# Optimization experiments

Measured on AMD Instinct MI355X. Metric: run time of the kernel, lower is better.

Reference implementation:

```python
import jax, jax.numpy as jnp
from jax import lax
import numpy as np

SR = 48000
NUM_BANDS = 12
IR_LEN = 32768          # reverb impulse-response length in samples
NUM_TAPS = 511          # bandpass FIR length for the noise filterbank
BS, CHS, T = 32, 2, 131072
EPS = 1e-8


def make_filterbank():
    """12-band windowed-sinc bandpass filterbank spanning 0..Nyquist."""
    n = np.arange(NUM_TAPS) - (NUM_TAPS - 1) / 2.0
    win = np.hamming(NUM_TAPS)
    filts = []
    for b in range(NUM_BANDS):
        lo = 0.5 * b / NUM_BANDS
        hi = 0.5 * (b + 1) / NUM_BANDS
        h = 2.0 * hi * np.sinc(2.0 * hi * n) - 2.0 * lo * np.sinc(2.0 * lo * n)
        filts.append(h * win)
    return np.stack(filts).astype(np.float32)  # (12, NUM_TAPS)


def _distortion(x, drive_db):
    # tanh waveshaper with dB drive gain
    return jnp.tanh(x * 10.0 ** (drive_db / 20.0))


def _compressor(x, thr, ratio, atk_ms, rel_ms, knee, makeup):
    # soft-knee gain computer in dB domain
    x_db = 20.0 * jnp.log10(jnp.abs(x) + EPS)          # (bs, chs, T)
    knee = jnp.maximum(knee, 1e-3)
    over = x_db - thr
    g_knee = x_db + (1.0 / ratio - 1.0) * (over + knee / 2.0) ** 2 / (2.0 * knee)
    g = jnp.where(2.0 * over < -knee, x_db,
                  jnp.where(2.0 * over > knee, thr + over / ratio, g_knee))
    gain_db = g - x_db                                  # desired gain reduction (<= 0)
    # per-sample attack/release one-pole envelope follower (sequential scan)
    alpha_a = jnp.exp(-1.0 / (SR * atk_ms / 1000.0))
    alpha_r = jnp.exp(-1.0 / (SR * rel_ms / 1000.0))
    g_t = jnp.moveaxis(gain_db, -1, 0)                  # (T, bs, chs)

    def step(prev, cur):
        alpha = jnp.where(cur < prev, alpha_a, alpha_r)  # attack when reduction grows
        new = alpha * prev + (1.0 - alpha) * cur
        return new, new

    _, smooth = lax.scan(step, jnp.zeros(g_t.shape[1:], x.dtype), g_t)
    smooth = jnp.moveaxis(smooth, 0, -1)                # (bs, chs, T)
    return x * 10.0 ** ((smooth + makeup) / 20.0)


def _reverb(x, band_gains, band_decays, mix, noise, fir_bank):
    bs, chs, seq = x.shape
    n = noise.reshape(bs * chs, NUM_BANDS, -1)          # (N, 12, IR_LEN+TAPS-1)
    # grouped conv: each band of noise filtered by its bandpass FIR
    filt = lax.conv_general_dilated(
        n, fir_bank[:, None, :], (1,), 'VALID',
        dimension_numbers=('NCH', 'OIH', 'NCH'),
        feature_group_count=NUM_BANDS)                  # (N, 12, IR_LEN)
    t = jnp.linspace(0.0, 1.0, IR_LEN, dtype=x.dtype)
    d = band_decays * 10.0 + 1.0
    env = jnp.exp(-d[:, None] * t[None, :])             # (12, IR_LEN) decay envelopes
    ir = jnp.mean(filt * (env * band_gains[:, None]), axis=1)  # (N, IR_LEN)
    ir = ir.reshape(bs, chs, IR_LEN)
    # FFT convolution of input with the synthesized IR
    nfft = seq + IR_LEN - 1
    wet = jnp.fft.irfft(jnp.fft.rfft(x, nfft) * jnp.fft.rfft(ir, nfft), nfft)[..., :seq]
    return (1.0 - mix) * x + mix * wet


def _forward(x, drive, thr, ratio, atk, rel, knee, makeup, mix,
             band_gains, band_decays, noise, fir_bank):
    x = _distortion(x, drive)
    x = _compressor(x, thr, ratio, atk, rel, knee, makeup)
    return _reverb(x, band_gains, band_decays, mix, noise, fir_bank)


def setup_inputs() -> dict:
    key = jax.random.key(0)
    k1, k2 = jax.random.split(key)
    return {
        "x": 0.5 * jax.random.normal(k1, (BS, CHS, T), jnp.float32),
        "drive": jnp.float32(5.0),
        "threshold_db": jnp.float32(-20.0),
        "ratio": jnp.float32(4.0),
        "attack_ms": jnp.float32(10.0),
        "release_ms": jnp.float32(50.0),
        "knee_db": jnp.float32(6.0),
        "makeup_gain_db": jnp.float32(0.0),
        "mix": jnp.float32(0.3),
        "band_gains": jnp.zeros((NUM_BANDS,), jnp.float32),
        "band_decays": 0.5 * jnp.ones((NUM_BANDS,), jnp.float32),
        "noise": jax.random.normal(k2, (BS, CHS, NUM_BANDS, IR_LEN + NUM_TAPS - 1), jnp.float32),
        "fir_bank": jnp.asarray(make_filterbank()),
    }


def reference(x, drive, threshold_db, ratio, attack_ms, release_ms, knee_db,
              makeup_gain_db, mix, band_gains, band_decays, noise, fir_bank):
    return _forward(x, drive, threshold_db, ratio, attack_ms, release_ms,
                    knee_db, makeup_gain_db, mix, band_gains, band_decays,
                    noise, fir_bank)
```

## Files before the change

### kernel.cpp

```cpp
#include <hip/hip_runtime.h>
#include <math.h>
#include <stdint.h>

#define NCHW    64
#define TLEN    131072
#define IRLEN   32768
#define NTAPS   511
#define NBANDS  12
#define NOISELEN (IRLEN + NTAPS - 1)

#define WUP     4096
#define CHK     512
#define NBLK2   (TLEN / CHK)
#define NQ      (TLEN / 4)
#define GRP     16

#define K10     0.16609640474436813f
#define DB2     6.0205999132796239f

__device__ __forceinline__ float fast_tanh(float z) {
    float az = fabsf(z);
    float e  = exp2f(az * 2.8853900817779268f);
    float r  = 1.0f - 2.0f / (e + 1.0f);
    return copysignf(r, z);
}

__device__ __forceinline__ float gain_db_one(float xs, float g, float thr,
                                             float q, float knee, float inv2k) {
    float y    = fast_tanh(xs * g);
    float a    = fabsf(y) + 1e-8f;
    float xdb  = __log2f(a) * DB2;
    float over = xdb - thr;
    float h    = over + 0.5f * knee;
    float gk   = q * h * h * inv2k;
    float t2   = 2.0f * over;
    return (t2 < -knee) ? 0.0f : ((t2 > knee) ? q * over : gk);
}

__device__ __forceinline__ float f4c(const float4& v, int s) {
    return s == 0 ? v.x : (s == 1 ? v.y : (s == 2 ? v.z : v.w));
}

__global__ __launch_bounds__(256) void k1_gain(
    const float* __restrict__ x,
    const float* __restrict__ p_drive, const float* __restrict__ p_thr,
    const float* __restrict__ p_ratio, const float* __restrict__ p_knee,
    const float* __restrict__ p_atk,   const float* __restrict__ p_rel,
    const float* __restrict__ band_gains,
    float4* __restrict__ q4, float* __restrict__ q1, float4* __restrict__ pq,
    int* __restrict__ flag)
{
    if (blockIdx.x == 0 && threadIdx.x == 0) {
        int f = 0;
        #pragma unroll
        for (int b = 0; b < NBANDS; ++b) f |= (band_gains[b] != 0.0f) ? 1 : 0;
        *flag = f;
    }
    __shared__ float S[64 * 65];
    int t0 = blockIdx.x * 64;
    int l  = threadIdx.x & 63;
    int w  = threadIdx.x >> 6;

    float g     = exp2f(p_drive[0] * K10);
    float thr   = p_thr[0];
    float knee  = fmaxf(p_knee[0], 1e-3f);
    float qr    = 1.0f / p_ratio[0] - 1.0f;
    float inv2k = 1.0f / (2.0f * knee);
    float aa    = expf(-1.0f / (48.0f * p_atk[0]));
    float ar    = expf(-1.0f / (48.0f * p_rel[0]));
    float omaa  = 1.0f - aa;
    float rho   = (1.0f - ar) / omaa;

    #pragma unroll
    for (int i = 0; i < 16; ++i) {
        int ch = w * 16 + i;
        float xv = x[(size_t)ch * TLEN + t0 + l];
        S[l * 65 + ch] = omaa * gain_db_one(xv, g, thr, qr, knee, inv2k);
    }
    __syncthreads();

    int ch = threadIdx.x & 63;
    int ql = threadIdx.x >> 6;
    #pragma unroll
    for (int k = 0; k < 4; ++k) {
        int qq = ql * 4 + k;
        int sb = qq * 4;
        float A0 = S[(sb + 0) * 65 + ch];
        float A1 = S[(sb + 1) * 65 + ch];
        float A2 = S[(sb + 2) * 65 + ch];
        float A3 = S[(sb + 3) * 65 + ch];
        float R0 = rho * A0, R1 = rho * A1, R2 = rho * A2, R3 = rho * A3;
        float i0 = A0, i1 = R0;
        float n0 = fmaf(aa, i0, A1);
        float n1 = fminf(fmaf(aa, i1, A1), fmaf(ar, i0, R1));
        float n2 = fmaf(ar, i1, R1);
        float m0 = fmaf(aa, n0, A2);
        float m1 = fminf(fmaf(aa, n1, A2), fmaf(ar, n0, R2));
        float m2 = fminf(fmaf(aa, n2, A2), fmaf(ar, n1, R2));
        float m3 = fmaf(ar, n2, R2);
        float o0 = fmaf(aa, m0, A3);
        float o1 = fminf(fmaf(aa, m1, A3), fmaf(ar, m0, R3));
        float o2 = fminf(fmaf(aa, m2, A3), fmaf(ar, m1, R3));
        float o3 = fminf(fmaf(aa, m3, A3), fmaf(ar, m2, R3));
        float o4 = fmaf(ar, m3, R3);
        size_t gi = (size_t)(blockIdx.x * 16 + qq) * 64 + ch;
        q4[gi] = make_float4(o0, o1, o2, o3);
        q1[gi] = o4;
        pq[gi] = make_float4(A0, A1, A2, A3);
    }
}

#define WSTEP(c4, c1s) { \
    float f0 = fmaf(s0, p, (c4).x); \
    float f1 = fmaf(s1, p, (c4).y); \
    float f2 = fmaf(s2, p, (c4).z); \
    float f3 = fmaf(s3, p, (c4).w); \
    float f4 = fmaf(s4, p, (c1s)); \
    p = fminf(fminf(fminf(f0, f1), f2), fminf(f3, f4)); \
}

#define ESTEP(Av, tl) { \
    float fa = fmaf(aa, p, (Av)); \
    float fr = fmaf(ar, p, rho * (Av)); \
    p = fminf(fa, fr); \
    Ssm[(tl) * 68 + lane] = p; \
}

#define APPLY(xv, tq, cq) { \
    float4 sm0 = *(const float4*)&Ssm[(4 * (tq) + 0) * 68 + (cq) * 4]; \
    float4 sm1 = *(const float4*)&Ssm[(4 * (tq) + 1) * 68 + (cq) * 4]; \
    float4 sm2 = *(const float4*)&Ssm[(4 * (tq) + 2) * 68 + (cq) * 4]; \
    float4 sm3 = *(const float4*)&Ssm[(4 * (tq) + 3) * 68 + (cq) * 4]; \
    _Pragma("unroll") \
    for (int cc = 0; cc < 4; ++cc) { \
        float c0 = fast_tanh(f4c(xv[cc], 0) * g) * exp2f((f4c(sm0, cc) + mk) * K10); \
        float c1 = fast_tanh(f4c(xv[cc], 1) * g) * exp2f((f4c(sm1, cc) + mk) * K10); \
        float c2 = fast_tanh(f4c(xv[cc], 2) * g) * exp2f((f4c(sm2, cc) + mk) * K10); \
        float c3 = fast_tanh(f4c(xv[cc], 3) * g) * exp2f((f4c(sm3, cc) + mk) * K10); \
        size_t oidx = (size_t)((cq) * 4 + cc) * TLEN + tb + 4 * (tq); \
        *(float4*)&out[oidx] = make_float4(dry * c0, dry * c1, dry * c2, dry * c3); \
        if (sflag) *(float4*)&comp[oidx] = make_float4(c0, c1, c2, c3); \
    } \
}

__global__ __launch_bounds__(256, 1) void k2_env(
    const float* __restrict__ x,
    const float4* __restrict__ q4, const float* __restrict__ q1,
    const float4* __restrict__ pq,
    const float* __restrict__ p_atk, const float* __restrict__ p_rel,
    const float* __restrict__ p_drive, const float* __restrict__ p_makeup,
    const float* __restrict__ p_mix, const int* __restrict__ flag,
    float* __restrict__ out, float* __restrict__ comp)
{
    __shared__ __attribute__((aligned(16))) float Ssm[128 * 68];
    __shared__ int sflag;
    int tid = threadIdx.x;
    if (tid == 0) sflag = *flag;

    int b  = blockIdx.x;
    int j  = ((b & 7) << 5) | (b >> 3);
    int te = j * CHK;
    int t0 = (j >= WUP / CHK) ? te - WUP : 0;
    int q0 = t0 >> 2, qe = te >> 2;
    int lane = tid & 63;

    float aa  = expf(-1.0f / (48.0f * p_atk[0]));
    float ar  = expf(-1.0f / (48.0f * p_rel[0]));
    float rho = (1.0f - ar) / (1.0f - aa);
    float s0 = aa * aa * aa * aa, s1 = aa * aa * aa * ar, s2 = aa * aa * ar * ar,
          s3 = aa * ar * ar * ar, s4 = ar * ar * ar * ar;
    float g   = exp2f(p_drive[0] * K10);
    float mk  = p_makeup[0];
    float mix = p_mix[0];
    float dry = 1.0f - mix;

    float p = 0.0f;

    if (tid < 64 && qe > q0) {
        float4 A4[GRP]; float A1v[GRP]; float4 B4[GRP]; float B1v[GRP];
        size_t base = (size_t)q0 * 64 + lane;
        #pragma unroll
        for (int u = 0; u < GRP; ++u) {
            A4[u]  = q4[base + (size_t)u * 64];
            A1v[u] = q1[base + (size_t)u * 64];
        }
        for (int gq = q0; gq < qe; gq += 2 * GRP) {
            size_t bb = (size_t)(gq + GRP) * 64 + lane;
            #pragma unroll
            for (int u = 0; u < GRP; ++u) {
                B4[u]  = q4[bb + (size_t)u * 64];
                B1v[u] = q1[bb + (size_t)u * 64];
            }
            #pragma unroll
            for (int u = 0; u < GRP; ++u) WSTEP(A4[u], A1v[u]);
            size_t ab = (size_t)(gq + 2 * GRP) * 64 + lane;
            #pragma unroll
            for (int u = 0; u < GRP; ++u) {
                A4[u]  = q4[ab + (size_t)u * 64];
                A1v[u] = q1[ab + (size_t)u * 64];
            }
            #pragma unroll
            for (int u = 0; u < GRP; ++u) WSTEP(B4[u], B1v[u]);
        }
    }

    int tqa = tid & 31,         cqa = tid >> 5;
    int tqb = (tid + 256) & 31, cqb = (tid + 256) >> 5;

    for (int r = 0; r < 4; ++r) {
        int tb = te + r * 128;
        float4 xva[4], xvb[4];
        #pragma unroll
        for (int cc = 0; cc < 4; ++cc) {
            xva[cc] = *(const float4*)&x[(size_t)(cqa * 4 + cc) * TLEN + tb + 4 * tqa];
            xvb[cc] = *(const float4*)&x[(size_t)(cqb * 4 + cc) * TLEN + tb + 4 * tqb];
        }
        if (tid < 64) {
            float4 C4[GRP], D4[GRP];
            size_t eb = (size_t)(qe + r * 32) * 64 + lane;
            #pragma unroll
            for (int u = 0; u < GRP; ++u) C4[u] = pq[eb + (size_t)u * 64];
            #pragma unroll
            for (int u = 0; u < GRP; ++u) D4[u] = pq[eb + (size_t)(u + GRP) * 64];
            #pragma unroll
            for (int u = 0; u < GRP; ++u) {
                ESTEP(C4[u].x, u * 4 + 0); ESTEP(C4[u].y, u * 4 + 1);
                ESTEP(C4[u].z, u * 4 + 2); ESTEP(C4[u].w, u * 4 + 3);
            }
            #pragma unroll
            for (int u = 0; u < GRP; ++u) {
                int t4 = (u + GRP) * 4;
                ESTEP(D4[u].x, t4 + 0); ESTEP(D4[u].y, t4 + 1);
                ESTEP(D4[u].z, t4 + 2); ESTEP(D4[u].w, t4 + 3);
            }
        }
        __syncthreads();
        APPLY(xva, tqa, cqa);
        APPLY(xvb, tqb, cqb);
        __syncthreads();
    }
}

__global__ __launch_bounds__(256) void k4_ir(
    const float* __restrict__ noise, const float* __restrict__ fir,
    const float* __restrict__ gains, const float* __restrict__ decays,
    const int* __restrict__ flag, float* __restrict__ ir)
{
    __shared__ int sflag;
    if (threadIdx.x == 0) sflag = *flag;
    __syncthreads();
    if (!sflag) return;
    __shared__ float sf[NBANDS * NTAPS];
    for (int i = threadIdx.x; i < NBANDS * NTAPS; i += 256) sf[i] = fir[i];
    __syncthreads();
    size_t total  = (size_t)NCHW * IRLEN;
    size_t stride = (size_t)gridDim.x * 256;
    for (size_t idx = blockIdx.x * 256 + threadIdx.x; idx < total; idx += stride) {
        int nch = (int)(idx >> 15);
        int n   = (int)(idx & (IRLEN - 1));
        float tl  = n * (1.0f / (IRLEN - 1));
        float acc = 0.0f;
        for (int bb = 0; bb < NBANDS; ++bb) {
            float gb = gains[bb];
            if (gb == 0.0f) continue;
            float env = expf(-(decays[bb] * 10.0f + 1.0f) * tl) * gb;
            const float* np_ = noise + ((size_t)nch * NBANDS + bb) * NOISELEN + n;
            const float* fb  = sf + bb * NTAPS;
            float s = 0.0f;
            for (int k = 0; k < NTAPS; ++k) s = fmaf(np_[k], fb[k], s);
            acc = fmaf(env, s, acc);
        }
        ir[idx] = acc * (1.0f / NBANDS);
    }
}

__global__ __launch_bounds__(256) void k5_wet(
    const float* __restrict__ comp, const float* __restrict__ ir,
    const float* __restrict__ p_mix, const int* __restrict__ flag,
    float* __restrict__ out)
{
    __shared__ int sflag;
    if (threadIdx.x == 0) sflag = *flag;
    __syncthreads();
    if (!sflag) return;
    float mix = p_mix[0];
    size_t total  = (size_t)NCHW * TLEN;
    size_t stride = (size_t)gridDim.x * 256;
    for (size_t idx = blockIdx.x * 256 + threadIdx.x; idx < total; idx += stride) {
        int nch = (int)(idx >> 17);
        int t   = (int)(idx & (TLEN - 1));
        const float* c   = comp + (size_t)nch * TLEN;
        const float* irp = ir + (size_t)nch * IRLEN;
        int kmax = (t < IRLEN - 1) ? t : (IRLEN - 1);
        float s = 0.0f;
        for (int k = 0; k <= kmax; ++k) s = fmaf(irp[k], c[t - k], s);
        out[idx] += mix * s;
    }
}

extern "C" void kernel_launch(void* const* d_in, const int* in_sizes, int n_in,
                              void* d_out, int out_size, void* d_ws, size_t ws_size,
                              hipStream_t stream)
{
    const float* x      = (const float*)d_in[0];
    const float* drive  = (const float*)d_in[1];
    const float* thr    = (const float*)d_in[2];
    const float* ratio  = (const float*)d_in[3];
    const float* atk    = (const float*)d_in[4];
    const float* rel    = (const float*)d_in[5];
    const float* knee   = (const float*)d_in[6];
    const float* makeup = (const float*)d_in[7];
    const float* mix    = (const float*)d_in[8];
    const float* bg     = (const float*)d_in[9];
    const float* bd     = (const float*)d_in[10];
    const float* noise  = (const float*)d_in[11];
    const float* fir    = (const float*)d_in[12];
    float* out = (float*)d_out;

    char*  w    = (char*)d_ws;
    int*   flag = (int*)w;
    float* q4f  = (float*)(w + 16);
    float* q1f  = q4f + (size_t)NQ * 256;
    float* pqf  = q1f + (size_t)NQ * 64;
    float* cmp  = pqf + (size_t)NQ * 256;
    float* ir   = cmp + (size_t)NCHW * TLEN;

    k1_gain<<<TLEN / 64, 256, 0, stream>>>(x, drive, thr, ratio, knee, atk, rel,
                                           bg, (float4*)q4f, q1f, (float4*)pqf, flag);
    k2_env<<<NBLK2, 256, 0, stream>>>(x, (const float4*)q4f, q1f, (const float4*)pqf,
                                      atk, rel, drive, makeup, mix, flag, out, cmp);
    k4_ir<<<256, 256, 0, stream>>>(noise, fir, bg, bd, flag, ir);
    k5_wet<<<256, 256, 0, stream>>>(cmp, ir, mix, flag, out);
}
```

Before: 253.3 us.

## Stream warmup coefficients via async LDS ring and recompute gain in-block

The compressor warmup scan in k2 now loads its per-quad coefficients through a triple-buffered global_load_lds ring with explicit vmcnt waits, replacing register double-buffering. The per-sample gain values (pq) are no longer written by k1; the other three waves recompute them from x into double-buffered LDS tiles while wave 0 runs the scan. The tail q1 values are also packed as float4 per block. This removes a large intermediate write and read and overlaps gain computation with the serial scan, at the cost of more LDS use, redundant gain math, and a fragile hand-set waitcnt.

```diff
diff --git a/kernel.cpp b/kernel.cpp
--- a/kernel.cpp
+++ b/kernel.cpp
@@ -13,7 +13,10 @@
 #define CHK     512
 #define NBLK2   (TLEN / CHK)
 #define NQ      (TLEN / 4)
-#define GRP     16
+
+#define GRPQ    16
+#define SLOTB   (GRPQ * 1024 + (GRPQ / 4) * 1024)
+#define AFLOATS (128 * 68)
 
 #define K10     0.16609640474436813f
 #define DB2     6.0205999132796239f
@@ -47,7 +50,7 @@
     const float* __restrict__ p_ratio, const float* __restrict__ p_knee,
     const float* __restrict__ p_atk,   const float* __restrict__ p_rel,
     const float* __restrict__ band_gains,
-    float4* __restrict__ q4, float* __restrict__ q1, float4* __restrict__ pq,
+    float4* __restrict__ q4, float4* __restrict__ q1t,
     int* __restrict__ flag)
 {
     if (blockIdx.x == 0 && threadIdx.x == 0) {
@@ -81,6 +84,7 @@
 
     int ch = threadIdx.x & 63;
     int ql = threadIdx.x >> 6;
+    float o4v[4];
     #pragma unroll
     for (int k = 0; k < 4; ++k) {
         int qq = ql * 4 + k;
@@ -102,12 +106,12 @@
         float o1 = fminf(fmaf(aa, m1, A3), fmaf(ar, m0, R3));
         float o2 = fminf(fmaf(aa, m2, A3), fmaf(ar, m1, R3));
         float o3 = fminf(fmaf(aa, m3, A3), fmaf(ar, m2, R3));
-        float o4 = fmaf(ar, m3, R3);
+        o4v[k]   = fmaf(ar, m3, R3);
         size_t gi = (size_t)(blockIdx.x * 16 + qq) * 64 + ch;
         q4[gi] = make_float4(o0, o1, o2, o3);
-        q1[gi] = o4;
-        pq[gi] = make_float4(A0, A1, A2, A3);
-    }
+    }
+    q1t[((size_t)blockIdx.x * 4 + ql) * 64 + ch] =
+        make_float4(o4v[0], o4v[1], o4v[2], o4v[3]);
 }
 
 #define WSTEP(c4, c1s) { \
@@ -119,18 +123,27 @@
     p = fminf(fminf(fminf(f0, f1), f2), fminf(f3, f4)); \
 }
 
-#define ESTEP(Av, tl) { \
-    float fa = fmaf(aa, p, (Av)); \
-    float fr = fmaf(ar, p, rho * (Av)); \
-    p = fminf(fa, fr); \
-    Ssm[(tl) * 68 + lane] = p; \
-}
-
-#define APPLY(xv, tq, cq) { \
-    float4 sm0 = *(const float4*)&Ssm[(4 * (tq) + 0) * 68 + (cq) * 4]; \
-    float4 sm1 = *(const float4*)&Ssm[(4 * (tq) + 1) * 68 + (cq) * 4]; \
-    float4 sm2 = *(const float4*)&Ssm[(4 * (tq) + 2) * 68 + (cq) * 4]; \
-    float4 sm3 = *(const float4*)&Ssm[(4 * (tq) + 3) * 68 + (cq) * 4]; \
+#define ISSUE_GROUP(gg, slot) { \
+    const char* s4_ = (const char*)q4g + (((size_t)(q0 + (gg) * GRPQ)) << 10) + lane * 16; \
+    char* dp_ = ring + (slot) * SLOTB; \
+    _Pragma("unroll") \
+    for (int k_ = 0; k_ < 16; ++k_) \
+        __builtin_amdgcn_global_load_lds( \
+            (const __attribute__((address_space(1))) void*)(s4_ + (k_ << 10)), \
+            (__attribute__((address_space(3))) void*)(dp_ + (k_ << 10)), 16, 0, 0); \
+    const char* s1_ = (const char*)q1g + (((size_t)((q0 >> 2) + (gg) * 4)) << 10) + lane * 16; \
+    _Pragma("unroll") \
+    for (int k_ = 0; k_ < 4; ++k_) \
+        __builtin_amdgcn_global_load_lds( \
+            (const __attribute__((address_space(1))) void*)(s1_ + (k_ << 10)), \
+            (__attribute__((address_space(3))) void*)(dp_ + 16384 + (k_ << 10)), 16, 0, 0); \
+}
+
+#define APPLY(B, xv, tq, cq) { \
+    float4 sm0 = *(const float4*)&(B)[(4 * (tq) + 0) * 68 + (cq) * 4]; \
+    float4 sm1 = *(const float4*)&(B)[(4 * (tq) + 1) * 68 + (cq) * 4]; \
+    float4 sm2 = *(const float4*)&(B)[(4 * (tq) + 2) * 68 + (cq) * 4]; \
+    float4 sm3 = *(const float4*)&(B)[(4 * (tq) + 3) * 68 + (cq) * 4]; \
     _Pragma("unroll") \
     for (int cc = 0; cc < 4; ++cc) { \
         float c0 = fast_tanh(f4c(xv[cc], 0) * g) * exp2f((f4c(sm0, cc) + mk) * K10); \
@@ -145,15 +158,20 @@
 
 __global__ __launch_bounds__(256, 1) void k2_env(
     const float* __restrict__ x,
-    const float4* __restrict__ q4, const float* __restrict__ q1,
-    const float4* __restrict__ pq,
-    const float* __restrict__ p_atk, const float* __restrict__ p_rel,
-    const float* __restrict__ p_drive, const float* __restrict__ p_makeup,
-    const float* __restrict__ p_mix, const int* __restrict__ flag,
+    const float* __restrict__ q4g, const float* __restrict__ q1g,
+    const float* __restrict__ p_drive, const float* __restrict__ p_thr,
+    const float* __restrict__ p_ratio, const float* __restrict__ p_knee,
+    const float* __restrict__ p_atk,  const float* __restrict__ p_rel,
+    const float* __restrict__ p_makeup, const float* __restrict__ p_mix,
+    const int* __restrict__ flag,
     float* __restrict__ out, float* __restrict__ comp)
 {
-    __shared__ __attribute__((aligned(16))) float Ssm[128 * 68];
+    __shared__ __attribute__((aligned(16))) char smem[3 * SLOTB + 2 * AFLOATS * 4];
     __shared__ int sflag;
+    char*  ring = smem;
+    float* Ab0  = (float*)(smem + 3 * SLOTB);
+    float* Ab1  = Ab0 + AFLOATS;
+
     int tid = threadIdx.x;
     if (tid == 0) sflag = *flag;
 
@@ -163,46 +181,59 @@
     int t0 = (j >= WUP / CHK) ? te - WUP : 0;
     int q0 = t0 >> 2, qe = te >> 2;
     int lane = tid & 63;
+    int wv   = tid >> 6;
 
     float aa  = expf(-1.0f / (48.0f * p_atk[0]));
     float ar  = expf(-1.0f / (48.0f * p_rel[0]));
-    float rho = (1.0f - ar) / (1.0f - aa);
+    float omaa = 1.0f - aa;
+    float rho  = (1.0f - ar) / omaa;
     float s0 = aa * aa * aa * aa, s1 = aa * aa * aa * ar, s2 = aa * aa * ar * ar,
           s3 = aa * ar * ar * ar, s4 = ar * ar * ar * ar;
-    float g   = exp2f(p_drive[0] * K10);
+    float g     = exp2f(p_drive[0] * K10);
+    float thr   = p_thr[0];
+    float knee  = fmaxf(p_knee[0], 1e-3f);
+    float qr    = 1.0f / p_ratio[0] - 1.0f;
+    float inv2k = 1.0f / (2.0f * knee);
     float mk  = p_makeup[0];
     float mix = p_mix[0];
     float dry = 1.0f - mix;
 
     float p = 0.0f;
-
-    if (tid < 64 && qe > q0) {
-        float4 A4[GRP]; float A1v[GRP]; float4 B4[GRP]; float B1v[GRP];
-        size_t base = (size_t)q0 * 64 + lane;
-        #pragma unroll
-        for (int u = 0; u < GRP; ++u) {
-            A4[u]  = q4[base + (size_t)u * 64];
-            A1v[u] = q1[base + (size_t)u * 64];
-        }
-        for (int gq = q0; gq < qe; gq += 2 * GRP) {
-            size_t bb = (size_t)(gq + GRP) * 64 + lane;
-            #pragma unroll
-            for (int u = 0; u < GRP; ++u) {
-                B4[u]  = q4[bb + (size_t)u * 64];
-                B1v[u] = q1[bb + (size_t)u * 64];
+    int ng = (qe - q0) / GRPQ;
+
+    if (wv == 0) {
+        if (ng > 0) {
+            ISSUE_GROUP(0, 0);
+            ISSUE_GROUP((ng > 1 ? 1 : 0), 1);
+            int sl = 0;
+            for (int gq = 0; gq < ng; ++gq) {
+                int gi = (gq + 2 < ng) ? gq + 2 : ng - 1;
+                int sli = sl + 2; if (sli >= 3) sli -= 3;
+                ISSUE_GROUP(gi, sli);
+                asm volatile("s_waitcnt vmcnt(40)" ::: "memory");
+                __builtin_amdgcn_sched_barrier(0);
+                const char* slotp = ring + sl * SLOTB;
+                #pragma unroll
+                for (int kk = 0; kk < 4; ++kk) {
+                    float4 c1v = *(const float4*)(slotp + 16384 + (kk << 10) + lane * 16);
+                    #pragma unroll
+                    for (int jj = 0; jj < 4; ++jj) {
+                        float4 c4 = *(const float4*)(slotp + ((kk * 4 + jj) << 10) + lane * 16);
+                        WSTEP(c4, f4c(c1v, jj));
+                    }
+                }
+                sl = (sl == 2) ? 0 : sl + 1;
             }
-            #pragma unroll
-            for (int u = 0; u < GRP; ++u) WSTEP(A4[u], A1v[u]);
-            size_t ab = (size_t)(gq + 2 * GRP) * 64 + lane;
-            #pragma unroll
-            for (int u = 0; u < GRP; ++u) {
-                A4[u]  = q4[ab + (size_t)u * 64];
-                A1v[u] = q1[ab + (size_t)u * 64];
-            }
-            #pragma unroll
-            for (int u = 0; u < GRP; ++u) WSTEP(B4[u], B1v[u]);
-        }
-    }
+        }
+    } else {
+        int tid192 = tid - 64;
+        for (int c = tid192; c < 8192; c += 192) {
+            int t = c & 127, ch = c >> 7;
+            float xv = x[(size_t)ch * TLEN + te + t];
+            Ab0[t * 68 + ch] = omaa * gain_db_one(xv, g, thr, qr, knee, inv2k);
+        }
+    }
+    __syncthreads();
 
     int tqa = tid & 31,         cqa = tid >> 5;
     int tqb = (tid + 256) & 31, cqb = (tid + 256) >> 5;
@@ -215,28 +246,29 @@
             xva[cc] = *(const float4*)&x[(size_t)(cqa * 4 + cc) * TLEN + tb + 4 * tqa];
             xvb[cc] = *(const float4*)&x[(size_t)(cqb * 4 + cc) * TLEN + tb + 4 * tqb];
         }
-        if (tid < 64) {
-            float4 C4[GRP], D4[GRP];
-            size_t eb = (size_t)(qe + r * 32) * 64 + lane;
-            #pragma unroll
-            for (int u = 0; u < GRP; ++u) C4[u] = pq[eb + (size_t)u * 64];
-            #pragma unroll
-            for (int u = 0; u < GRP; ++u) D4[u] = pq[eb + (size_t)(u + GRP) * 64];
-            #pragma unroll
-            for (int u = 0; u < GRP; ++u) {
-                ESTEP(C4[u].x, u * 4 + 0); ESTEP(C4[u].y, u * 4 + 1);
-                ESTEP(C4[u].z, u * 4 + 2); ESTEP(C4[u].w, u * 4 + 3);
+        float* Bc = (r & 1) ? Ab1 : Ab0;
+        if (wv == 0) {
+            float* Bl = Bc + lane;
+            #pragma unroll 8
+            for (int t = 0; t < 128; ++t) {
+                float a  = Bl[t * 68];
+                float fa = fmaf(aa, p, a);
+                float fr = fmaf(ar, p, rho * a);
+                p = fminf(fa, fr);
+                Bl[t * 68] = p;
             }
-            #pragma unroll
-            for (int u = 0; u < GRP; ++u) {
-                int t4 = (u + GRP) * 4;
-                ESTEP(D4[u].x, t4 + 0); ESTEP(D4[u].y, t4 + 1);
-                ESTEP(D4[u].z, t4 + 2); ESTEP(D4[u].w, t4 + 3);
+        } else if (r < 3) {
+            float* Bn = (r & 1) ? Ab0 : Ab1;
+            int tid192 = tid - 64;
+            for (int c = tid192; c < 8192; c += 192) {
+                int t = c & 127, ch = c >> 7;
+                float xv = x[(size_t)ch * TLEN + tb + 128 + t];
+                Bn[t * 68 + ch] = omaa * gain_db_one(xv, g, thr, qr, knee, inv2k);
             }
         }
         __syncthreads();
-        APPLY(xva, tqa, cqa);
-        APPLY(xvb, tqb, cqb);
+        APPLY(Bc, xva, tqa, cqa);
+        APPLY(Bc, xvb, tqb, cqb);
         __syncthreads();
     }
 }
@@ -321,14 +353,13 @@
     int*   flag = (int*)w;
     float* q4f  = (float*)(w + 16);
     float* q1f  = q4f + (size_t)NQ * 256;
-    float* pqf  = q1f + (size_t)NQ * 64;
-    float* cmp  = pqf + (size_t)NQ * 256;
+    float* cmp  = q1f + (size_t)NQ * 64;
     float* ir   = cmp + (size_t)NCHW * TLEN;
 
     k1_gain<<<TLEN / 64, 256, 0, stream>>>(x, drive, thr, ratio, knee, atk, rel,
-                                           bg, (float4*)q4f, q1f, (float4*)pqf, flag);
-    k2_env<<<NBLK2, 256, 0, stream>>>(x, (const float4*)q4f, q1f, (const float4*)pqf,
-                                      atk, rel, drive, makeup, mix, flag, out, cmp);
+                                           bg, (float4*)q4f, (float4*)q1f, flag);
+    k2_env<<<NBLK2, 256, 0, stream>>>(x, q4f, q1f, drive, thr, ratio, knee,
+                                      atk, rel, makeup, mix, flag, out, cmp);
     k4_ir<<<256, 256, 0, stream>>>(noise, fir, bg, bd, flag, ir);
     k5_wet<<<256, 256, 0, stream>>>(cmp, ir, mix, flag, out);
 }
```

Measured after the change: 308.0 us. 1.22x slower.

## Stage envelope warmup scan through double-buffered LDS filled by producer waves

Applied to the files above, without the earlier changes.

The warmup scan in k2_env used to be run by one wave, which loaded its q4/q1 operands straight from global memory into registers. Now the other three waves act as producers: they copy 32-quad groups into a double-buffered shared-memory tile while wave 0 scans the previous tile. k1 also writes the trailing o4 values as a transposed float4 array, so each group's q1 terms can be fetched with vector loads. The goal is to hide global-load latency on the serial scan, at the cost of 80KB of extra LDS and a block-wide barrier on every group.

```diff
diff --git a/kernel.cpp b/kernel.cpp
--- a/kernel.cpp
+++ b/kernel.cpp
@@ -13,7 +13,11 @@
 #define CHK     512
 #define NBLK2   (TLEN / CHK)
 #define NQ      (TLEN / 4)
-#define GRP     16
+
+#define TQUADS  32
+#define TROWS   40
+#define TBYTES  (TROWS * 1024)
+#define PROWS   14
 
 #define K10     0.16609640474436813f
 #define DB2     6.0205999132796239f
@@ -47,7 +51,7 @@
     const float* __restrict__ p_ratio, const float* __restrict__ p_knee,
     const float* __restrict__ p_atk,   const float* __restrict__ p_rel,
     const float* __restrict__ band_gains,
-    float4* __restrict__ q4, float* __restrict__ q1, float4* __restrict__ pq,
+    float4* __restrict__ q4, float4* __restrict__ q1t, float4* __restrict__ pq,
     int* __restrict__ flag)
 {
     if (blockIdx.x == 0 && threadIdx.x == 0) {
@@ -81,6 +85,7 @@
 
     int ch = threadIdx.x & 63;
     int ql = threadIdx.x >> 6;
+    float o4v[4];
     #pragma unroll
     for (int k = 0; k < 4; ++k) {
         int qq = ql * 4 + k;
@@ -102,12 +107,13 @@
         float o1 = fminf(fmaf(aa, m1, A3), fmaf(ar, m0, R3));
         float o2 = fminf(fmaf(aa, m2, A3), fmaf(ar, m1, R3));
         float o3 = fminf(fmaf(aa, m3, A3), fmaf(ar, m2, R3));
-        float o4 = fmaf(ar, m3, R3);
+        o4v[k]   = fmaf(ar, m3, R3);
         size_t gi = (size_t)(blockIdx.x * 16 + qq) * 64 + ch;
         q4[gi] = make_float4(o0, o1, o2, o3);
-        q1[gi] = o4;
         pq[gi] = make_float4(A0, A1, A2, A3);
     }
+    q1t[((size_t)blockIdx.x * 4 + ql) * 64 + ch] =
+        make_float4(o4v[0], o4v[1], o4v[2], o4v[3]);
 }
 
 #define WSTEP(c4, c1s) { \
@@ -143,15 +149,37 @@
     } \
 }
 
+__device__ __forceinline__ const char* row_src(const char* q4b, const char* q1b,
+                                               int q0, int k, int r, int lane) {
+    return (r < TQUADS)
+        ? q4b + (((size_t)(q0 + k * TQUADS + r)) << 10) + lane * 16
+        : q1b + (((size_t)((q0 >> 2) + k * 8 + (r - TQUADS))) << 10) + lane * 16;
+}
+
+#define PLOAD(k_) { \
+    _Pragma("unroll") \
+    for (int i_ = 0; i_ < PROWS; ++i_) { \
+        int r_ = pr0 + 3 * i_; \
+        if (r_ < TROWS) Rg[i_] = *(const float4*)row_src(q4b, q1b, q0, (k_), r_, lane); \
+    } }
+#define PWRITE(bsel) { \
+    _Pragma("unroll") \
+    for (int i_ = 0; i_ < PROWS; ++i_) { \
+        int r_ = pr0 + 3 * i_; \
+        if (r_ < TROWS) \
+            *(float4*)(buf + (bsel) * TBYTES + r_ * 1024 + lane * 16) = Rg[i_]; \
+    } }
+
 __global__ __launch_bounds__(256, 1) void k2_env(
     const float* __restrict__ x,
-    const float4* __restrict__ q4, const float* __restrict__ q1,
+    const float* __restrict__ q4g, const float* __restrict__ q1g,
     const float4* __restrict__ pq,
     const float* __restrict__ p_atk, const float* __restrict__ p_rel,
     const float* __restrict__ p_drive, const float* __restrict__ p_makeup,
     const float* __restrict__ p_mix, const int* __restrict__ flag,
     float* __restrict__ out, float* __restrict__ comp)
 {
+    __shared__ __attribute__((aligned(16))) char  buf[2 * TBYTES];
     __shared__ __attribute__((aligned(16))) float Ssm[128 * 68];
     __shared__ int sflag;
     int tid = threadIdx.x;
@@ -163,6 +191,7 @@
     int t0 = (j >= WUP / CHK) ? te - WUP : 0;
     int q0 = t0 >> 2, qe = te >> 2;
     int lane = tid & 63;
+    int wv   = tid >> 6;
 
     float aa  = expf(-1.0f / (48.0f * p_atk[0]));
     float ar  = expf(-1.0f / (48.0f * p_rel[0]));
@@ -174,33 +203,39 @@
     float mix = p_mix[0];
     float dry = 1.0f - mix;
 
+    const char* q4b = (const char*)q4g;
+    const char* q1b = (const char*)q1g;
+
     float p = 0.0f;
-
-    if (tid < 64 && qe > q0) {
-        float4 A4[GRP]; float A1v[GRP]; float4 B4[GRP]; float B1v[GRP];
-        size_t base = (size_t)q0 * 64 + lane;
-        #pragma unroll
-        for (int u = 0; u < GRP; ++u) {
-            A4[u]  = q4[base + (size_t)u * 64];
-            A1v[u] = q1[base + (size_t)u * 64];
-        }
-        for (int gq = q0; gq < qe; gq += 2 * GRP) {
-            size_t bb = (size_t)(gq + GRP) * 64 + lane;
-            #pragma unroll
-            for (int u = 0; u < GRP; ++u) {
-                B4[u]  = q4[bb + (size_t)u * 64];
-                B1v[u] = q1[bb + (size_t)u * 64];
+    int ng = (qe - q0) >> 5;
+
+    if (ng > 0) {
+        int pr0 = wv - 1;
+        float4 Rg[PROWS];
+        if (wv > 0) {
+            PLOAD(0);
+            PWRITE(0);
+            PLOAD((1 < ng ? 1 : 0));
+        }
+        __syncthreads();
+        for (int k = 0; k < ng; ++k) {
+            if (wv == 0) {
+                const char* bp = buf + (k & 1) * TBYTES;
+                #pragma unroll
+                for (int kk = 0; kk < 8; ++kk) {
+                    float4 c1v = *(const float4*)(bp + 32768 + (kk << 10) + lane * 16);
+                    #pragma unroll
+                    for (int jj = 0; jj < 4; ++jj) {
+                        float4 c4 = *(const float4*)(bp + ((kk * 4 + jj) << 10) + lane * 16);
+                        WSTEP(c4, f4c(c1v, jj));
+                    }
+                }
+            } else if (k + 1 < ng) {
+                PWRITE((k + 1) & 1);
+                int nk = (k + 2 < ng) ? k + 2 : ng - 1;
+                PLOAD(nk);
             }
-            #pragma unroll
-            for (int u = 0; u < GRP; ++u) WSTEP(A4[u], A1v[u]);
-            size_t ab = (size_t)(gq + 2 * GRP) * 64 + lane;
-            #pragma unroll
-            for (int u = 0; u < GRP; ++u) {
-                A4[u]  = q4[ab + (size_t)u * 64];
-                A1v[u] = q1[ab + (size_t)u * 64];
-            }
-            #pragma unroll
-            for (int u = 0; u < GRP; ++u) WSTEP(B4[u], B1v[u]);
+            __syncthreads();
         }
     }
 
@@ -216,20 +251,20 @@
             xvb[cc] = *(const float4*)&x[(size_t)(cqb * 4 + cc) * TLEN + tb + 4 * tqb];
         }
         if (tid < 64) {
-            float4 C4[GRP], D4[GRP];
+            float4 C4[16], D4[16];
             size_t eb = (size_t)(qe + r * 32) * 64 + lane;
             #pragma unroll
-            for (int u = 0; u < GRP; ++u) C4[u] = pq[eb + (size_t)u * 64];
+            for (int u = 0; u < 16; ++u) C4[u] = pq[eb + (size_t)u * 64];
             #pragma unroll
-            for (int u = 0; u < GRP; ++u) D4[u] = pq[eb + (size_t)(u + GRP) * 64];
+            for (int u = 0; u < 16; ++u) D4[u] = pq[eb + (size_t)(u + 16) * 64];
             #pragma unroll
-            for (int u = 0; u < GRP; ++u) {
+            for (int u = 0; u < 16; ++u) {
                 ESTEP(C4[u].x, u * 4 + 0); ESTEP(C4[u].y, u * 4 + 1);
                 ESTEP(C4[u].z, u * 4 + 2); ESTEP(C4[u].w, u * 4 + 3);
             }
             #pragma unroll
-            for (int u = 0; u < GRP; ++u) {
-                int t4 = (u + GRP) * 4;
+            for (int u = 0; u < 16; ++u) {
+                int t4 = (u + 16) * 4;
                 ESTEP(D4[u].x, t4 + 0); ESTEP(D4[u].y, t4 + 1);
                 ESTEP(D4[u].z, t4 + 2); ESTEP(D4[u].w, t4 + 3);
             }
@@ -326,8 +361,9 @@
     float* ir   = cmp + (size_t)NCHW * TLEN;
 
     k1_gain<<<TLEN / 64, 256, 0, stream>>>(x, drive, thr, ratio, knee, atk, rel,
-                                           bg, (float4*)q4f, q1f, (float4*)pqf, flag);
-    k2_env<<<NBLK2, 256, 0, stream>>>(x, (const float4*)q4f, q1f, (const float4*)pqf,
+                                           bg, (float4*)q4f, (float4*)q1f,
+                                           (float4*)pqf, flag);
+    k2_env<<<NBLK2, 256, 0, stream>>>(x, q4f, q1f, (const float4*)pqf,
                                       atk, rel, drive, makeup, mix, flag, out, cmp);
     k4_ir<<<256, 256, 0, stream>>>(noise, fir, bg, bd, flag, ir);
     k5_wet<<<256, 256, 0, stream>>>(cmp, ir, mix, flag, out);
```

Result: slower. 349.0 us (+37.8%).

## Recompute gain in env kernel with warp-specialized double-buffered LDS pipeline

Applied to the files above, without the earlier changes.

k1 no longer writes the per-sample gain array pq. k2 now recomputes the gain and the tanh value from x in three producer waves that fill double-buffered shared memory, while wave 0 runs the sequential envelope scan on the previous buffer. The chunk size doubles to 1024, so there are half as many blocks and the warm-up overhead is amortised over more samples. This removes a large global write and read round trip and the duplicated tanh. The cost is more shared memory, fewer blocks (128) to occupy the GPU, and a scan that now reads LDS serially.

```diff
diff --git a/kernel.cpp b/kernel.cpp
--- a/kernel.cpp
+++ b/kernel.cpp
@@ -10,10 +10,12 @@
 #define NOISELEN (IRLEN + NTAPS - 1)
 
 #define WUP     4096
-#define CHK     512
+#define CHK     1024
 #define NBLK2   (TLEN / CHK)
 #define NQ      (TLEN / 4)
 #define GRP     16
+
+#define AFLOATS (128 * 68)
 
 #define K10     0.16609640474436813f
 #define DB2     6.0205999132796239f
@@ -47,7 +49,7 @@
     const float* __restrict__ p_ratio, const float* __restrict__ p_knee,
     const float* __restrict__ p_atk,   const float* __restrict__ p_rel,
     const float* __restrict__ band_gains,
-    float4* __restrict__ q4, float* __restrict__ q1, float4* __restrict__ pq,
+    float4* __restrict__ q4, float* __restrict__ q1,
     int* __restrict__ flag)
 {
     if (blockIdx.x == 0 && threadIdx.x == 0) {
@@ -106,7 +108,6 @@
         size_t gi = (size_t)(blockIdx.x * 16 + qq) * 64 + ch;
         q4[gi] = make_float4(o0, o1, o2, o3);
         q1[gi] = o4;
-        pq[gi] = make_float4(A0, A1, A2, A3);
     }
 }
 
@@ -119,24 +120,37 @@
     p = fminf(fminf(fminf(f0, f1), f2), fminf(f3, f4)); \
 }
 
-#define ESTEP(Av, tl) { \
-    float fa = fmaf(aa, p, (Av)); \
-    float fr = fmaf(ar, p, rho * (Av)); \
-    p = fminf(fa, fr); \
-    Ssm[(tl) * 68 + lane] = p; \
-}
-
-#define APPLY(xv, tq, cq) { \
-    float4 sm0 = *(const float4*)&Ssm[(4 * (tq) + 0) * 68 + (cq) * 4]; \
-    float4 sm1 = *(const float4*)&Ssm[(4 * (tq) + 1) * 68 + (cq) * 4]; \
-    float4 sm2 = *(const float4*)&Ssm[(4 * (tq) + 2) * 68 + (cq) * 4]; \
-    float4 sm3 = *(const float4*)&Ssm[(4 * (tq) + 3) * 68 + (cq) * 4]; \
+#define FILLA(Ba, Ya, tb_) { \
+    for (int c_ = tid - 64; c_ < 8192; c_ += 192) { \
+        int t_ = c_ & 127, ch_ = c_ >> 7; \
+        float xv_  = x[(size_t)ch_ * TLEN + (tb_) + t_]; \
+        float y_   = fast_tanh(xv_ * g); \
+        float a_   = fabsf(y_) + 1e-8f; \
+        float xdb_ = __log2f(a_) * DB2; \
+        float ov_  = xdb_ - thr; \
+        float h_   = ov_ + 0.5f * knee; \
+        float gk_  = qr * h_ * h_ * inv2k; \
+        float t2_  = 2.0f * ov_; \
+        float gd_  = (t2_ < -knee) ? 0.0f : ((t2_ > knee) ? qr * ov_ : gk_); \
+        (Ba)[t_ * 68 + ch_] = omaa * gd_; \
+        (Ya)[t_ * 68 + ch_] = y_; \
+    } }
+
+#define APPLY(B, Y, tq, cq) { \
+    float4 sm0 = *(const float4*)&(B)[(4 * (tq) + 0) * 68 + (cq) * 4]; \
+    float4 sm1 = *(const float4*)&(B)[(4 * (tq) + 1) * 68 + (cq) * 4]; \
+    float4 sm2 = *(const float4*)&(B)[(4 * (tq) + 2) * 68 + (cq) * 4]; \
+    float4 sm3 = *(const float4*)&(B)[(4 * (tq) + 3) * 68 + (cq) * 4]; \
+    float4 yv0 = *(const float4*)&(Y)[(4 * (tq) + 0) * 68 + (cq) * 4]; \
+    float4 yv1 = *(const float4*)&(Y)[(4 * (tq) + 1) * 68 + (cq) * 4]; \
+    float4 yv2 = *(const float4*)&(Y)[(4 * (tq) + 2) * 68 + (cq) * 4]; \
+    float4 yv3 = *(const float4*)&(Y)[(4 * (tq) + 3) * 68 + (cq) * 4]; \
     _Pragma("unroll") \
     for (int cc = 0; cc < 4; ++cc) { \
-        float c0 = fast_tanh(f4c(xv[cc], 0) * g) * exp2f((f4c(sm0, cc) + mk) * K10); \
-        float c1 = fast_tanh(f4c(xv[cc], 1) * g) * exp2f((f4c(sm1, cc) + mk) * K10); \
-        float c2 = fast_tanh(f4c(xv[cc], 2) * g) * exp2f((f4c(sm2, cc) + mk) * K10); \
-        float c3 = fast_tanh(f4c(xv[cc], 3) * g) * exp2f((f4c(sm3, cc) + mk) * K10); \
+        float c0 = f4c(yv0, cc) * exp2f((f4c(sm0, cc) + mk) * K10); \
+        float c1 = f4c(yv1, cc) * exp2f((f4c(sm1, cc) + mk) * K10); \
+        float c2 = f4c(yv2, cc) * exp2f((f4c(sm2, cc) + mk) * K10); \
+        float c3 = f4c(yv3, cc) * exp2f((f4c(sm3, cc) + mk) * K10); \
         size_t oidx = (size_t)((cq) * 4 + cc) * TLEN + tb + 4 * (tq); \
         *(float4*)&out[oidx] = make_float4(dry * c0, dry * c1, dry * c2, dry * c3); \
         if (sflag) *(float4*)&comp[oidx] = make_float4(c0, c1, c2, c3); \
@@ -146,97 +160,102 @@
 __global__ __launch_bounds__(256, 1) void k2_env(
     const float* __restrict__ x,
     const float4* __restrict__ q4, const float* __restrict__ q1,
-    const float4* __restrict__ pq,
-    const float* __restrict__ p_atk, const float* __restrict__ p_rel,
-    const float* __restrict__ p_drive, const float* __restrict__ p_makeup,
-    const float* __restrict__ p_mix, const int* __restrict__ flag,
+    const float* __restrict__ p_drive, const float* __restrict__ p_thr,
+    const float* __restrict__ p_ratio, const float* __restrict__ p_knee,
+    const float* __restrict__ p_atk,  const float* __restrict__ p_rel,
+    const float* __restrict__ p_makeup, const float* __restrict__ p_mix,
+    const int* __restrict__ flag,
     float* __restrict__ out, float* __restrict__ comp)
 {
-    __shared__ __attribute__((aligned(16))) float Ssm[128 * 68];
+    __shared__ __attribute__((aligned(16))) float Ab0[AFLOATS];
+    __shared__ __attribute__((aligned(16))) float Ab1[AFLOATS];
+    __shared__ __attribute__((aligned(16))) float Yb0[AFLOATS];
+    __shared__ __attribute__((aligned(16))) float Yb1[AFLOATS];
     __shared__ int sflag;
     int tid = threadIdx.x;
     if (tid == 0) sflag = *flag;
 
     int b  = blockIdx.x;
-    int j  = ((b & 7) << 5) | (b >> 3);
+    int j  = ((b & 7) << 4) | (b >> 3);
     int te = j * CHK;
     int t0 = (j >= WUP / CHK) ? te - WUP : 0;
     int q0 = t0 >> 2, qe = te >> 2;
     int lane = tid & 63;
+    int wv   = tid >> 6;
 
     float aa  = expf(-1.0f / (48.0f * p_atk[0]));
     float ar  = expf(-1.0f / (48.0f * p_rel[0]));
-    float rho = (1.0f - ar) / (1.0f - aa);
+    float omaa = 1.0f - aa;
+    float rho  = (1.0f - ar) / omaa;
     float s0 = aa * aa * aa * aa, s1 = aa * aa * aa * ar, s2 = aa * aa * ar * ar,
           s3 = aa * ar * ar * ar, s4 = ar * ar * ar * ar;
-    float g   = exp2f(p_drive[0] * K10);
+    float g     = exp2f(p_drive[0] * K10);
+    float thr   = p_thr[0];
+    float knee  = fmaxf(p_knee[0], 1e-3f);
+    float qr    = 1.0f / p_ratio[0] - 1.0f;
+    float inv2k = 1.0f / (2.0f * knee);
     float mk  = p_makeup[0];
     float mix = p_mix[0];
     float dry = 1.0f - mix;
 
     float p = 0.0f;
 
-    if (tid < 64 && qe > q0) {
-        float4 A4[GRP]; float A1v[GRP]; float4 B4[GRP]; float B1v[GRP];
-        size_t base = (size_t)q0 * 64 + lane;
-        #pragma unroll
-        for (int u = 0; u < GRP; ++u) {
-            A4[u]  = q4[base + (size_t)u * 64];
-            A1v[u] = q1[base + (size_t)u * 64];
-        }
-        for (int gq = q0; gq < qe; gq += 2 * GRP) {
-            size_t bb = (size_t)(gq + GRP) * 64 + lane;
+    if (wv == 0) {
+        if (qe > q0) {
+            float4 A4[GRP]; float A1v[GRP]; float4 B4[GRP]; float B1v[GRP];
+            size_t base = (size_t)q0 * 64 + lane;
             #pragma unroll
             for (int u = 0; u < GRP; ++u) {
-                B4[u]  = q4[bb + (size_t)u * 64];
-                B1v[u] = q1[bb + (size_t)u * 64];
+                A4[u]  = q4[base + (size_t)u * 64];
+                A1v[u] = q1[base + (size_t)u * 64];
             }
-            #pragma unroll
-            for (int u = 0; u < GRP; ++u) WSTEP(A4[u], A1v[u]);
-            size_t ab = (size_t)(gq + 2 * GRP) * 64 + lane;
-            #pragma unroll
-            for (int u = 0; u < GRP; ++u) {
-                A4[u]  = q4[ab + (size_t)u * 64];
-                A1v[u] = q1[ab + (size_t)u * 64];
+            for (int gq = q0; gq < qe; gq += 2 * GRP) {
+                size_t bb = (size_t)(gq + GRP) * 64 + lane;
+                #pragma unroll
+                for (int u = 0; u < GRP; ++u) {
+                    B4[u]  = q4[bb + (size_t)u * 64];
+                    B1v[u] = q1[bb + (size_t)u * 64];
+                }
+                #pragma unroll
+                for (int u = 0; u < GRP; ++u) WSTEP(A4[u], A1v[u]);
+                size_t ab = (size_t)(gq + 2 * GRP) * 64 + lane;
+                #pragma unroll
+                for (int u = 0; u < GRP; ++u) {
+                    A4[u]  = q4[ab + (size_t)u * 64];
+                    A1v[u] = q1[ab + (size_t)u * 64];
+                }
+                #pragma unroll
+                for (int u = 0; u < GRP; ++u) WSTEP(B4[u], B1v[u]);
             }
-            #pragma unroll
-            for (int u = 0; u < GRP; ++u) WSTEP(B4[u], B1v[u]);
         }
-    }
+    } else {
+        FILLA(Ab0, Yb0, te);
+    }
+    __syncthreads();
 
     int tqa = tid & 31,         cqa = tid >> 5;
     int tqb = (tid + 256) & 31, cqb = (tid + 256) >> 5;
 
-    for (int r = 0; r < 4; ++r) {
+    for (int r = 0; r < CHK / 128; ++r) {
         int tb = te + r * 128;
-        float4 xva[4], xvb[4];
-        #pragma unroll
-        for (int cc = 0; cc < 4; ++cc) {
-            xva[cc] = *(const float4*)&x[(size_t)(cqa * 4 + cc) * TLEN + tb + 4 * tqa];
-            xvb[cc] = *(const float4*)&x[(size_t)(cqb * 4 + cc) * TLEN + tb + 4 * tqb];
-        }
-        if (tid < 64) {
-            float4 C4[GRP], D4[GRP];
-            size_t eb = (size_t)(qe + r * 32) * 64 + lane;
-            #pragma unroll
-            for (int u = 0; u < GRP; ++u) C4[u] = pq[eb + (size_t)u * 64];
-            #pragma unroll
-            for (int u = 0; u < GRP; ++u) D4[u] = pq[eb + (size_t)(u + GRP) * 64];
-            #pragma unroll
-            for (int u = 0; u < GRP; ++u) {
-                ESTEP(C4[u].x, u * 4 + 0); ESTEP(C4[u].y, u * 4 + 1);
-                ESTEP(C4[u].z, u * 4 + 2); ESTEP(C4[u].w, u * 4 + 3);
+        float* Bc = (r & 1) ? Ab1 : Ab0;
+        float* Yc = (r & 1) ? Yb1 : Yb0;
+        if (wv == 0) {
+            float* Bl = Bc + lane;
+            #pragma unroll 8
+            for (int t = 0; t < 128; ++t) {
+                float a  = Bl[t * 68];
+                float fa = fmaf(aa, p, a);
+                float fr = fmaf(ar, p, rho * a);
+                p = fminf(fa, fr);
+                Bl[t * 68] = p;
             }
-            #pragma unroll
-            for (int u = 0; u < GRP; ++u) {
-                int t4 = (u + GRP) * 4;
-                ESTEP(D4[u].x, t4 + 0); ESTEP(D4[u].y, t4 + 1);
-                ESTEP(D4[u].z, t4 + 2); ESTEP(D4[u].w, t4 + 3);
-            }
+        } else if (r < CHK / 128 - 1) {
+            FILLA((r & 1) ? Ab0 : Ab1, (r & 1) ? Yb0 : Yb1, tb + 128);
         }
         __syncthreads();
-        APPLY(xva, tqa, cqa);
-        APPLY(xvb, tqb, cqb);
+        APPLY(Bc, Yc, tqa, cqa);
+        APPLY(Bc, Yc, tqb, cqb);
         __syncthreads();
     }
 }
@@ -321,14 +340,14 @@
     int*   flag = (int*)w;
     float* q4f  = (float*)(w + 16);
     float* q1f  = q4f + (size_t)NQ * 256;
-    float* pqf  = q1f + (size_t)NQ * 64;
-    float* cmp  = pqf + (size_t)NQ * 256;
+    float* cmp  = q1f + (size_t)NQ * 64;
     float* ir   = cmp + (size_t)NCHW * TLEN;
 
     k1_gain<<<TLEN / 64, 256, 0, stream>>>(x, drive, thr, ratio, knee, atk, rel,
-                                           bg, (float4*)q4f, q1f, (float4*)pqf, flag);
-    k2_env<<<NBLK2, 256, 0, stream>>>(x, (const float4*)q4f, q1f, (const float4*)pqf,
-                                      atk, rel, drive, makeup, mix, flag, out, cmp);
+                                           bg, (float4*)q4f, q1f, flag);
+    k2_env<<<NBLK2, 256, 0, stream>>>(x, (const float4*)q4f, q1f,
+                                      drive, thr, ratio, knee, atk, rel,
+                                      makeup, mix, flag, out, cmp);
     k4_ir<<<256, 256, 0, stream>>>(noise, fir, bg, bd, flag, ir);
     k5_wet<<<256, 256, 0, stream>>>(cmp, ir, mix, flag, out);
 }
```

After: 353.2 us. 1.39x slower.
